# Optimization experiments

Hardware: AMD Instinct MI355X
Metric: run time of the kernel (lower is better)

## Reference

```python
import jax, jax.numpy as jnp
import numpy as np

TAU = 0.2  # temperature

def setup_inputs() -> dict:
    key = jax.random.key(0)
    k1, k2, k3 = jax.random.split(key, 3)
    query = jax.random.normal(k1, (8192, 128), dtype=jnp.float32)
    pos = jax.random.normal(k2, (8192, 128), dtype=jnp.float32)
    neg = jax.random.normal(k3, (16384, 128), dtype=jnp.float32)
    return {"query": query, "pos": pos, "neg": neg}

def reference(query, pos, neg):
    # scores: [N, M] = query @ neg^T / tau
    scores = jnp.einsum('nd,md->nm', query, neg) / TAU
    # positive logits: [N]
    pos_logit = jnp.sum(query * pos, axis=-1) / TAU
    # loss = mean_n( logsumexp_m(scores) - pos_logit )
    lse = jax.scipy.special.logsumexp(scores, axis=-1)
    return jnp.mean(lse - pos_logit)
```

## Files before the change

kernel.cpp:

```cpp
#include <hip/hip_runtime.h>
#include <cstdint>

#define NQ    8192
#define NNEG  16384
#define DIM   128
#define SPLIT 16
#define CHUNK (NNEG / SPLIT)
#define K_SCALE 7.2134752044448169f
#define LN2     0.69314718055994531f

typedef __attribute__((ext_vector_type(8))) int   i32x8;
typedef __attribute__((ext_vector_type(4))) float f32x4;

union U8 { i32x8 v; int4 h[2]; };

__device__ inline void async_load16(const void* g, void* l) {
    __builtin_amdgcn_global_load_lds(
        (const __attribute__((address_space(1))) void*)g,
        (__attribute__((address_space(3))) void*)l, 16, 0, 0);
}

__device__ inline float waveReduceSum(float v) {
#pragma unroll
    for (int m = 32; m >= 1; m >>= 1) v += __shfl_xor(v, m, 64);
    return v;
}

__global__ __launch_bounds__(256) void iw_prep(
    const float* __restrict__ q, const float* __restrict__ p,
    const float* __restrict__ neg,
    unsigned char* __restrict__ qb8, unsigned char* __restrict__ nb8,
    float* __restrict__ out)
{
    const int tid = threadIdx.x;
    const int t = blockIdx.x * 256 + tid;
    constexpr int QT = NQ * DIM / 8;
    if (t < QT) {
        const float4* q4 = (const float4*)q;
        float4 v0 = q4[t * 2], v1 = q4[t * 2 + 1];
        int w0 = __builtin_amdgcn_cvt_pk_fp8_f32(v0.x * K_SCALE, v0.y * K_SCALE, 0, false);
        w0     = __builtin_amdgcn_cvt_pk_fp8_f32(v0.z * K_SCALE, v0.w * K_SCALE, w0, true);
        int w1 = __builtin_amdgcn_cvt_pk_fp8_f32(v1.x * K_SCALE, v1.y * K_SCALE, 0, false);
        w1     = __builtin_amdgcn_cvt_pk_fp8_f32(v1.z * K_SCALE, v1.w * K_SCALE, w1, true);
        ((int2*)qb8)[t] = make_int2(w0, w1);
        const float4* p4 = (const float4*)p;
        float4 p0 = p4[t * 2], p1 = p4[t * 2 + 1];
        float acc = fmaf(v0.x, p0.x, fmaf(v0.y, p0.y, fmaf(v0.z, p0.z, v0.w * p0.w)));
        acc = fmaf(v1.x, p1.x, fmaf(v1.y, p1.y, fmaf(v1.z, p1.z, fmaf(v1.w, p1.w, acc))));
        acc = waveReduceSum(acc);
        __shared__ float red[4];
        if ((tid & 63) == 0) red[tid >> 6] = acc;
        __syncthreads();
        if (tid == 0) {
            float s = red[0] + red[1] + red[2] + red[3];
            atomicAdd(out, s * (-1.0f / (0.2f * (float)NQ)));
        }
    } else {
        int j = t - QT;
        const float4* n4 = (const float4*)neg;
        float4 v0 = n4[j * 2], v1 = n4[j * 2 + 1];
        int w0 = __builtin_amdgcn_cvt_pk_fp8_f32(v0.x, v0.y, 0, false);
        w0     = __builtin_amdgcn_cvt_pk_fp8_f32(v0.z, v0.w, w0, true);
        int w1 = __builtin_amdgcn_cvt_pk_fp8_f32(v1.x, v1.y, 0, false);
        w1     = __builtin_amdgcn_cvt_pk_fp8_f32(v1.z, v1.w, w1, true);
        ((int2*)nb8)[j] = make_int2(w0, w1);
    }
}

__global__ __launch_bounds__(256, 4) void iw_main(
    const unsigned char* __restrict__ qb8, const unsigned char* __restrict__ nb8,
    float2* __restrict__ partial)
{
    constexpr int BM = 128, BN = 64, NIT = CHUNK / BN;
    __shared__ alignas(16) unsigned char n_lds[2 * BN * DIM];

    const int tid  = threadIdx.x;
    const int lane = tid & 63;
    const int w    = tid >> 6;
    const int quad = lane >> 4;
    const int c0   = lane & 15;

    const int row0   = blockIdx.x * BM;
    const int nbase0 = blockIdx.y * CHUNK;

    U8 afrag[2];
#pragma unroll
    for (int rs = 0; rs < 2; ++rs) {
        const int qrow = row0 + w * 32 + rs * 16 + c0;
        const int4* pa = reinterpret_cast<const int4*>(qb8 + (size_t)qrow * DIM + quad * 32);
        afrag[rs].h[0] = pa[0];
        afrag[rs].h[1] = pa[1];
    }

    int srcoff[2], dstoff[2];
#pragma unroll
    for (int j = 0; j < 2; ++j) {
        int L  = (w * 2 + j) * 64 + lane;
        int h  = L & 1, G = L >> 1;
        int r  = G >> 2;
        int kb = (G & 3) ^ (r & 3);
        srcoff[j] = r * DIM + kb * 32 + h * 16;
        dstoff[j] = (w * 2 + j) * 1024;
    }
#pragma unroll
    for (int j = 0; j < 2; ++j)
        async_load16(nb8 + (size_t)nbase0 * DIM + srcoff[j], n_lds + dstoff[j]);
    __syncthreads();

    float m_s[2][4], l_s[2][4];
#pragma unroll
    for (int rs = 0; rs < 2; ++rs)
#pragma unroll
        for (int i = 0; i < 4; ++i) { m_s[rs][i] = -1e30f; l_s[rs][i] = 0.f; }

    const f32x4 zero4 = {0.f, 0.f, 0.f, 0.f};

    for (int it = 0; it < NIT; ++it) {
        const int buf = (it & 1) * (BN * DIM);
        if (it + 1 < NIT) {
            const unsigned char* src = nb8 + (size_t)(nbase0 + (it + 1) * BN) * DIM;
            const int nbuf = ((it + 1) & 1) * (BN * DIM);
#pragma unroll
            for (int j = 0; j < 2; ++j)
                async_load16(src + srcoff[j], n_lds + nbuf + dstoff[j]);
        }

        f32x4 acc[2][4];
#pragma unroll
        for (int ns = 0; ns < 4; ++ns) {
            int c  = ns * 16 + c0;
            int g0 = (c << 2) + (quad ^ (c & 3));
            const int4* pb = reinterpret_cast<const int4*>(n_lds + buf + g0 * 32);
            U8 b;
            b.h[0] = pb[0];
            b.h[1] = pb[1];
            acc[0][ns] = __builtin_amdgcn_mfma_scale_f32_16x16x128_f8f6f4(
                afrag[0].v, b.v, zero4, 0, 0, 0, 127, 0, 127);
            acc[1][ns] = __builtin_amdgcn_mfma_scale_f32_16x16x128_f8f6f4(
                afrag[1].v, b.v, zero4, 0, 0, 0, 127, 0, 127);
        }

#pragma unroll
        for (int rs = 0; rs < 2; ++rs) {
#pragma unroll
            for (int i = 0; i < 4; ++i) {
                float y0 = acc[rs][0][i], y1 = acc[rs][1][i];
                float y2 = acc[rs][2][i], y3 = acc[rs][3][i];
                float mx = fmaxf(fmaxf(y0, y1), fmaxf(y2, y3));
                float m0 = m_s[rs][i];
                float nm = fmaxf(m0, mx);
                float t  = __builtin_amdgcn_exp2f(y0 - nm) + __builtin_amdgcn_exp2f(y1 - nm)
                         + __builtin_amdgcn_exp2f(y2 - nm) + __builtin_amdgcn_exp2f(y3 - nm);
                l_s[rs][i] = l_s[rs][i] * __builtin_amdgcn_exp2f(m0 - nm) + t;
                m_s[rs][i] = nm;
            }
        }
        __syncthreads();
    }

#pragma unroll
    for (int rs = 0; rs < 2; ++rs) {
#pragma unroll
        for (int i = 0; i < 4; ++i) {
            float m = m_s[rs][i], l = l_s[rs][i];
#pragma unroll
            for (int s = 1; s < 16; s <<= 1) {
                float om = __shfl_xor(m, s, 64);
                float ol = __shfl_xor(l, s, 64);
                float nm = fmaxf(m, om);
                l = l * __builtin_amdgcn_exp2f(m - nm) + ol * __builtin_amdgcn_exp2f(om - nm);
                m = nm;
            }
            if (c0 == 0) {
                int grow = row0 + w * 32 + rs * 16 + quad * 4 + i;
                partial[(size_t)blockIdx.y * NQ + grow] = make_float2(m, l);
            }
        }
    }
}

__global__ __launch_bounds__(256) void iw_merge(
    const float2* __restrict__ partial, float* __restrict__ out)
{
    const int tid = threadIdx.x;
    const int row = blockIdx.x * 256 + tid;
    float M = -1e30f, L = 0.f;
#pragma unroll
    for (int c = 0; c < SPLIT; ++c) {
        float2 p = partial[(size_t)c * NQ + row];
        float nm = fmaxf(M, p.x);
        L = L * __builtin_amdgcn_exp2f(M - nm) + p.y * __builtin_amdgcn_exp2f(p.x - nm);
        M = nm;
    }
    float lse = LN2 * (M + __log2f(L));
    float v = lse * (1.0f / (float)NQ);
    v = waveReduceSum(v);
    __shared__ float red[4];
    if ((tid & 63) == 0) red[tid >> 6] = v;
    __syncthreads();
    if (tid == 0) atomicAdd(out, red[0] + red[1] + red[2] + red[3]);
}

extern "C" void kernel_launch(void* const* d_in, const int* in_sizes, int n_in,
                              void* d_out, int out_size, void* d_ws, size_t ws_size,
                              hipStream_t stream) {
    const float* q   = (const float*)d_in[0];
    const float* pos = (const float*)d_in[1];
    const float* neg = (const float*)d_in[2];
    float* out = (float*)d_out;

    unsigned char* qb8 = (unsigned char*)d_ws;
    unsigned char* nb8 = qb8 + (size_t)NQ * DIM;
    float2* partial    = (float2*)(nb8 + (size_t)NNEG * DIM);

    hipMemsetAsync(out, 0, sizeof(float), stream);
    iw_prep <<<1536, 256, 0, stream>>>(q, pos, neg, qb8, nb8, out);
    iw_main <<<dim3(NQ / 128, SPLIT), 256, 0, stream>>>(qb8, nb8, partial);
    iw_merge<<<32,   256, 0, stream>>>(partial, out);
}
```

Measured before the change: 112.6 us.

## Load negative fragments directly from global memory instead of staging through LDS

Removes the LDS double-buffered async staging of the fp8 negative tile and per-iteration block barriers; each wave now reads its MFMA B fragments straight from global memory into registers. This eliminates __syncthreads and LDS traffic but makes all four waves fetch the same tile redundantly through the cache hierarchy and drops explicit prefetching, exposing global load latency unless the compiler hoists loads.

```diff
diff --git a/kernel.cpp b/kernel.cpp
--- a/kernel.cpp
+++ b/kernel.cpp
@@ -13,12 +13,6 @@
 typedef __attribute__((ext_vector_type(4))) float f32x4;
 
 union U8 { i32x8 v; int4 h[2]; };
-
-__device__ inline void async_load16(const void* g, void* l) {
-    __builtin_amdgcn_global_load_lds(
-        (const __attribute__((address_space(1))) void*)g,
-        (__attribute__((address_space(3))) void*)l, 16, 0, 0);
-}
 
 __device__ inline float waveReduceSum(float v) {
 #pragma unroll
@@ -72,8 +66,6 @@
     float2* __restrict__ partial)
 {
     constexpr int BM = 128, BN = 64, NIT = CHUNK / BN;
-    __shared__ alignas(16) unsigned char n_lds[2 * BN * DIM];
-
     const int tid  = threadIdx.x;
     const int lane = tid & 63;
     const int w    = tid >> 6;
@@ -92,20 +84,8 @@
         afrag[rs].h[1] = pa[1];
     }
 
-    int srcoff[2], dstoff[2];
-#pragma unroll
-    for (int j = 0; j < 2; ++j) {
-        int L  = (w * 2 + j) * 64 + lane;
-        int h  = L & 1, G = L >> 1;
-        int r  = G >> 2;
-        int kb = (G & 3) ^ (r & 3);
-        srcoff[j] = r * DIM + kb * 32 + h * 16;
-        dstoff[j] = (w * 2 + j) * 1024;
-    }
-#pragma unroll
-    for (int j = 0; j < 2; ++j)
-        async_load16(nb8 + (size_t)nbase0 * DIM + srcoff[j], n_lds + dstoff[j]);
-    __syncthreads();
+    const int4* bptr = reinterpret_cast<const int4*>(
+        nb8 + (size_t)(nbase0 + c0) * DIM + quad * 32);
 
     float m_s[2][4], l_s[2][4];
 #pragma unroll
@@ -116,28 +96,21 @@
     const f32x4 zero4 = {0.f, 0.f, 0.f, 0.f};
 
     for (int it = 0; it < NIT; ++it) {
-        const int buf = (it & 1) * (BN * DIM);
-        if (it + 1 < NIT) {
-            const unsigned char* src = nb8 + (size_t)(nbase0 + (it + 1) * BN) * DIM;
-            const int nbuf = ((it + 1) & 1) * (BN * DIM);
+        const int4* pb = bptr + (size_t)it * 512;
+        U8 b[4];
 #pragma unroll
-            for (int j = 0; j < 2; ++j)
-                async_load16(src + srcoff[j], n_lds + nbuf + dstoff[j]);
+        for (int ns = 0; ns < 4; ++ns) {
+            b[ns].h[0] = pb[ns * 128];
+            b[ns].h[1] = pb[ns * 128 + 1];
         }
 
         f32x4 acc[2][4];
 #pragma unroll
         for (int ns = 0; ns < 4; ++ns) {
-            int c  = ns * 16 + c0;
-            int g0 = (c << 2) + (quad ^ (c & 3));
-            const int4* pb = reinterpret_cast<const int4*>(n_lds + buf + g0 * 32);
-            U8 b;
-            b.h[0] = pb[0];
-            b.h[1] = pb[1];
             acc[0][ns] = __builtin_amdgcn_mfma_scale_f32_16x16x128_f8f6f4(
-                afrag[0].v, b.v, zero4, 0, 0, 0, 127, 0, 127);
+                afrag[0].v, b[ns].v, zero4, 0, 0, 0, 127, 0, 127);
             acc[1][ns] = __builtin_amdgcn_mfma_scale_f32_16x16x128_f8f6f4(
-                afrag[1].v, b.v, zero4, 0, 0, 0, 127, 0, 127);
+                afrag[1].v, b[ns].v, zero4, 0, 0, 0, 127, 0, 127);
         }
 
 #pragma unroll
@@ -146,16 +119,14 @@
             for (int i = 0; i < 4; ++i) {
                 float y0 = acc[rs][0][i], y1 = acc[rs][1][i];
                 float y2 = acc[rs][2][i], y3 = acc[rs][3][i];
-                float mx = fmaxf(fmaxf(y0, y1), fmaxf(y2, y3));
                 float m0 = m_s[rs][i];
-                float nm = fmaxf(m0, mx);
+                float nm = fmaxf(fmaxf(fmaxf(y0, y1), fmaxf(y2, y3)), m0);
                 float t  = __builtin_amdgcn_exp2f(y0 - nm) + __builtin_amdgcn_exp2f(y1 - nm)
                          + __builtin_amdgcn_exp2f(y2 - nm) + __builtin_amdgcn_exp2f(y3 - nm);
                 l_s[rs][i] = l_s[rs][i] * __builtin_amdgcn_exp2f(m0 - nm) + t;
                 m_s[rs][i] = nm;
             }
         }
-        __syncthreads();
     }
 
 #pragma unroll
```

New measurement: 139.0 us. 23.4% more time.
